# Kernel optimization log

Measured on AMD Instinct MI355X. Metric: run time of the kernel, lower is better.

Reference implementation:

```python
import jax, jax.numpy as jnp
import numpy as np

B, S, D, H, F = 2, 2048, 3072, 32, 8192
DH = D // H  # 96
EPS = 1e-5


def setup_inputs() -> dict:
    key = jax.random.key(0)
    ks = jax.random.split(key, 16)
    sd = 0.02
    inp = {
        "hidden_states": jax.random.normal(ks[0], (B, S, D), jnp.float32),
        "ln1_g": jnp.ones((D,), jnp.float32),
        "ln1_b": jnp.zeros((D,), jnp.float32),
        "Wq": jax.random.normal(ks[1], (D, H, DH), jnp.float32) * sd,
        "bq": jnp.zeros((H, DH), jnp.float32),
        "Wk": jax.random.normal(ks[2], (D, H, DH), jnp.float32) * sd,
        "bk": jnp.zeros((H, DH), jnp.float32),
        "Wv": jax.random.normal(ks[3], (D, H, DH), jnp.float32) * sd,
        "bv": jnp.zeros((H, DH), jnp.float32),
        "Wo": jax.random.normal(ks[4], (H, DH, D), jnp.float32) * sd,
        "bo": jnp.zeros((D,), jnp.float32),
        "ln2_g": jnp.ones((D,), jnp.float32),
        "ln2_b": jnp.zeros((D,), jnp.float32),
        "W1": jax.random.normal(ks[5], (D, F), jnp.float32) * sd,
        "b1": jnp.zeros((F,), jnp.float32),
        "W2": jax.random.normal(ks[6], (F, D), jnp.float32) * sd,
        "b2": jnp.zeros((D,), jnp.float32),
    }
    return inp


def _layernorm(x, g, b):
    m = jnp.mean(x, axis=-1, keepdims=True)
    v = jnp.mean(jnp.square(x - m), axis=-1, keepdims=True)
    return (x - m) * jax.lax.rsqrt(v + EPS) * g + b


def reference(hidden_states, ln1_g, ln1_b, Wq, bq, Wk, bk, Wv, bv, Wo, bo,
              ln2_g, ln2_b, W1, b1, W2, b2):
    # --- LN + self-attention + residual ---
    h = _layernorm(hidden_states, ln1_g, ln1_b)  # [B,S,D]
    q = jnp.einsum('bsd,dhk->bshk', h, Wq) + bq  # [B,S,H,DH]
    k = jnp.einsum('bsd,dhk->bshk', h, Wk) + bk
    v = jnp.einsum('bsd,dhk->bshk', h, Wv) + bv
    scale = 1.0 / np.sqrt(DH).astype(np.float32)
    scores = jnp.einsum('bshk,bthk->bhst', q, k) * scale  # [B,H,S,S]
    attn = jax.nn.softmax(scores, axis=-1)
    ctx = jnp.einsum('bhst,bthk->bshk', attn, v)  # [B,S,H,DH]
    attn_out = jnp.einsum('bshk,hkd->bsd', ctx, Wo) + bo
    h1 = hidden_states + attn_out
    # --- LN + MLP + residual ---
    h2 = _layernorm(h1, ln2_g, ln2_b)
    mlp = jax.nn.gelu(h2 @ W1 + b1, approximate=False) @ W2 + b2
    return h1 + mlp
```

## Files before the change

kernel.cpp:

```cpp
#include <hip/hip_runtime.h>
#include <math.h>

#define DEV __device__ __forceinline__

typedef __attribute__((ext_vector_type(8))) __bf16 bfrag;
typedef __attribute__((ext_vector_type(4))) float f4;
typedef __attribute__((ext_vector_type(8))) unsigned short u16x8;
typedef __attribute__((ext_vector_type(4))) unsigned short u16x4;

DEV unsigned short f2bf(float f) {
  unsigned u = __float_as_uint(f);
  u += 0x7fff + ((u >> 16) & 1);
  return (unsigned short)(u >> 16);
}

DEV void gload_lds16(const void* g, void* l) {
  __builtin_amdgcn_global_load_lds((const __attribute__((address_space(1))) void*)g,
                                   (__attribute__((address_space(3))) void*)l, 16, 0, 0);
}

template<int EPI, int OUTBF, int BIASROW>
__global__ __launch_bounds__(512, 2)
void gemm256(const unsigned short* __restrict__ A,
             const unsigned short* __restrict__ Bt,
             const float* __restrict__ bias,
             const float* __restrict__ res,
             void* __restrict__ outp,
             int M, int N, int K, int gm, int cm, int cn)
{
  __shared__ unsigned short As[2][256 * 64];
  __shared__ unsigned short Bs[2][256 * 64];

  const int tid = threadIdx.x;
  const int lane = tid & 63;
  const int wid = tid >> 6;
  const int wm = wid >> 2, wn = wid & 3;
  const int l15 = lane & 15, lg = lane >> 4;

  const int xcd = blockIdx.x & 7, idx = blockIdx.x >> 3;
  const int cgm = gm / cm;
  const int tm = (xcd % cgm) * cm + idx % cm;
  const int tn = (xcd / cgm) * cn + idx / cm;
  const long tM = (long)tm * 256, tN = (long)tn * 256;

  const int srow = tid >> 3;
  const int lslot = (tid & 7) ^ (srow & 7);
  const unsigned short* aSrc = A + (tM + srow) * (long)K + lslot * 8;
  const unsigned short* bSrc = Bt + (tN + srow) * (long)K + lslot * 8;
  const int NT = K >> 6;

  auto stA = [&](int t, int j) {
    gload_lds16(aSrc + (long)t * 64 + (long)j * 64 * K, &As[t & 1][j * 4096 + tid * 8]);
  };
  auto stB = [&](int t, int j) {
    gload_lds16(bSrc + (long)t * 64 + (long)j * 64 * K, &Bs[t & 1][j * 4096 + tid * 8]);
  };

#pragma unroll
  for (int j = 0; j < 4; ++j) stA(0, j);
#pragma unroll
  for (int j = 0; j < 4; ++j) stB(0, j);
  stA(1, 0); stA(1, 2);
#pragma unroll
  for (int j = 0; j < 4; ++j) stB(1, j);
  asm volatile("s_waitcnt vmcnt(6)" ::: "memory");
  __builtin_amdgcn_s_barrier();

  const int aRow = (wm * 128 + l15) * 64;
  const int bRow = (wn * 64 + l15) * 64;
  const int sx = l15 & 7;
  const int sl0 = ((0 + lg) ^ sx) * 8;
  const int sl1 = ((4 + lg) ^ sx) * 8;

  bfrag aF[4][2], bF[4][2];
  f4 acc[8][4] = {};

  int cur = 0;
  for (int t = 0; t < NT; ++t, cur ^= 1) {
    const unsigned short* Ac = As[cur];
    const unsigned short* Bc = Bs[cur];
    const bool s1 = (t + 1 < NT);
    const bool s2 = (t + 2 < NT);

#pragma unroll
    for (int m = 0; m < 4; ++m) {
      aF[m][0] = *(const bfrag*)&Ac[aRow + m * 1024 + sl0];
      aF[m][1] = *(const bfrag*)&Ac[aRow + m * 1024 + sl1];
    }
#pragma unroll
    for (int n = 0; n < 2; ++n) {
      bF[n][0] = *(const bfrag*)&Bc[bRow + n * 1024 + sl0];
      bF[n][1] = *(const bfrag*)&Bc[bRow + n * 1024 + sl1];
    }
    if (s1) { stA(t + 1, 1); stA(t + 1, 3); }
    __builtin_amdgcn_s_barrier();
    asm volatile("s_waitcnt lgkmcnt(0)" ::: "memory");
    __builtin_amdgcn_s_setprio(1);
#pragma unroll
    for (int m = 0; m < 4; ++m)
#pragma unroll
      for (int n = 0; n < 2; ++n) {
        acc[m][n] = __builtin_amdgcn_mfma_f32_16x16x32_bf16(aF[m][0], bF[n][0], acc[m][n], 0, 0, 0);
        acc[m][n] = __builtin_amdgcn_mfma_f32_16x16x32_bf16(aF[m][1], bF[n][1], acc[m][n], 0, 0, 0);
      }
    __builtin_amdgcn_s_setprio(0);
    __builtin_amdgcn_s_barrier();

#pragma unroll
    for (int n = 2; n < 4; ++n) {
      bF[n][0] = *(const bfrag*)&Bc[bRow + n * 1024 + sl0];
      bF[n][1] = *(const bfrag*)&Bc[bRow + n * 1024 + sl1];
    }
    if (s2) { stA(t + 2, 0); stA(t + 2, 2); }
    __builtin_amdgcn_s_barrier();
    asm volatile("s_waitcnt lgkmcnt(0)" ::: "memory");
    __builtin_amdgcn_s_setprio(1);
#pragma unroll
    for (int m = 0; m < 4; ++m)
#pragma unroll
      for (int n = 2; n < 4; ++n) {
        acc[m][n] = __builtin_amdgcn_mfma_f32_16x16x32_bf16(aF[m][0], bF[n][0], acc[m][n], 0, 0, 0);
        acc[m][n] = __builtin_amdgcn_mfma_f32_16x16x32_bf16(aF[m][1], bF[n][1], acc[m][n], 0, 0, 0);
      }
    __builtin_amdgcn_s_setprio(0);
    __builtin_amdgcn_s_barrier();

#pragma unroll
    for (int m = 0; m < 4; ++m) {
      aF[m][0] = *(const bfrag*)&Ac[aRow + 4096 + m * 1024 + sl0];
      aF[m][1] = *(const bfrag*)&Ac[aRow + 4096 + m * 1024 + sl1];
    }
    if (s2) { stB(t + 2, 0); stB(t + 2, 1); }
    __builtin_amdgcn_s_barrier();
    asm volatile("s_waitcnt lgkmcnt(0)" ::: "memory");
    __builtin_amdgcn_s_setprio(1);
#pragma unroll
    for (int m = 0; m < 4; ++m)
#pragma unroll
      for (int n = 0; n < 2; ++n) {
        acc[4 + m][n] = __builtin_amdgcn_mfma_f32_16x16x32_bf16(aF[m][0], bF[n][0], acc[4 + m][n], 0, 0, 0);
        acc[4 + m][n] = __builtin_amdgcn_mfma_f32_16x16x32_bf16(aF[m][1], bF[n][1], acc[4 + m][n], 0, 0, 0);
      }
    __builtin_amdgcn_s_setprio(0);
    __builtin_amdgcn_s_barrier();

    if (s2) { stB(t + 2, 2); stB(t + 2, 3); }
    __builtin_amdgcn_s_setprio(1);
#pragma unroll
    for (int m = 0; m < 4; ++m)
#pragma unroll
      for (int n = 2; n < 4; ++n) {
        acc[4 + m][n] = __builtin_amdgcn_mfma_f32_16x16x32_bf16(aF[m][0], bF[n][0], acc[4 + m][n], 0, 0, 0);
        acc[4 + m][n] = __builtin_amdgcn_mfma_f32_16x16x32_bf16(aF[m][1], bF[n][1], acc[4 + m][n], 0, 0, 0);
      }
    __builtin_amdgcn_s_setprio(0);
    if (s2)      asm volatile("s_waitcnt vmcnt(6)" ::: "memory");
    else if (s1) asm volatile("s_waitcnt vmcnt(0)" ::: "memory");
    __builtin_amdgcn_s_barrier();
  }

#pragma unroll
  for (int m = 0; m < 8; ++m) {
    const long row0 = tM + wm * 128 + m * 16 + lg * 4;
#pragma unroll
    for (int n = 0; n < 4; ++n) {
      const long col = tN + wn * 64 + n * 16 + l15;
      const float bc = BIASROW ? 0.f : bias[col];
#pragma unroll
      for (int e = 0; e < 4; ++e) {
        const long row = row0 + e;
        float v = acc[m][n][e] + (BIASROW ? bias[row] : bc);
        if constexpr (EPI == 1) v = 0.5f * v * (1.0f + erff(v * 0.70710678118654752f));
        if constexpr (EPI == 2) v += res[row * N + col];
        if constexpr (OUTBF) ((unsigned short*)outp)[row * N + col] = f2bf(v);
        else                 ((float*)outp)[row * N + col] = v;
      }
    }
  }
}

__global__ __launch_bounds__(256)
void ln_bf16(const float* __restrict__ x, const float* __restrict__ g,
             const float* __restrict__ b, unsigned short* __restrict__ out)
{
  __shared__ float red[4];
  const int tid = threadIdx.x;
  const long row = blockIdx.x;
  const float* xr = x + row * 3072;
  float4 v[3];
  float s = 0.f;
#pragma unroll
  for (int i = 0; i < 3; ++i) {
    v[i] = *(const float4*)&xr[i * 1024 + tid * 4];
    s += v[i].x + v[i].y + v[i].z + v[i].w;
  }
#pragma unroll
  for (int o = 32; o > 0; o >>= 1) s += __shfl_xor(s, o);
  if ((tid & 63) == 0) red[tid >> 6] = s;
  __syncthreads();
  s = red[0] + red[1] + red[2] + red[3];
  const float mean = s * (1.f / 3072.f);
  float vs = 0.f;
#pragma unroll
  for (int i = 0; i < 3; ++i) {
    const float dx = v[i].x - mean, dy = v[i].y - mean;
    const float dz = v[i].z - mean, dw = v[i].w - mean;
    vs += dx * dx + dy * dy + dz * dz + dw * dw;
  }
#pragma unroll
  for (int o = 32; o > 0; o >>= 1) vs += __shfl_xor(vs, o);
  __syncthreads();
  if ((tid & 63) == 0) red[tid >> 6] = vs;
  __syncthreads();
  vs = red[0] + red[1] + red[2] + red[3];
  const float rstd = rsqrtf(vs * (1.f / 3072.f) + 1e-5f);
#pragma unroll
  for (int i = 0; i < 3; ++i) {
    const int idx = i * 1024 + tid * 4;
    const float* vp = (const float*)&v[i];
    u16x4 o4;
#pragma unroll
    for (int c = 0; c < 4; ++c)
      o4[c] = f2bf((vp[c] - mean) * rstd * g[idx + c] + b[idx + c]);
    *(u16x4*)&out[row * 3072 + idx] = o4;
  }
}

__global__ __launch_bounds__(256)
void transpose_f32_bf16(const float* __restrict__ in, unsigned short* __restrict__ out,
                        int R, int C)
{
  __shared__ float tile[32][33];
  const int tx = threadIdx.x & 31, ty = threadIdx.x >> 5;
  const long r0 = (long)blockIdx.y * 32, cc0 = (long)blockIdx.x * 32;
#pragma unroll
  for (int i = 0; i < 4; ++i)
    tile[ty + 8 * i][tx] = in[(r0 + ty + 8 * i) * C + cc0 + tx];
  __syncthreads();
#pragma unroll
  for (int i = 0; i < 4; ++i)
    out[(cc0 + ty + 8 * i) * R + r0 + tx] = f2bf(tile[tx][ty + 8 * i]);
}

__global__ __launch_bounds__(256, 3)
void attn_fwd(const unsigned short* __restrict__ qk,
              const unsigned short* __restrict__ vT,
              unsigned short* __restrict__ ctx)
{
  __shared__ unsigned short Qs[64 * 104];
  __shared__ unsigned short Ks[64 * 104];
  __shared__ unsigned short Vt[96 * 72];
  __shared__ unsigned short Ps[4 * 16 * 72];
  const int tid = threadIdx.x;
  const int lane = tid & 63;
  const int w = tid >> 6;
  const int l15 = lane & 15, lg = lane >> 4;
  const int bid = (blockIdx.x & 7) * 256 + (blockIdx.x >> 3);
  const int qb = bid & 31;
  const int h = (bid >> 5) & 31;
  const int b = bid >> 10;
  const long qkbase = ((long)b * 2048) * 6144 + h * 96;
  const long obase  = ((long)b * 2048) * 3072 + h * 96;
  const long vbase  = (long)(h * 96) * 4096 + (long)b * 2048;
  const int qbase = qb * 64;

#pragma unroll
  for (int i = 0; i < 3; ++i) {
    const int c = tid + i * 256;
    const int r = c / 12, c8 = (c % 12) * 8;
    *(u16x8*)&Qs[r * 104 + c8] = *(const u16x8*)&qk[qkbase + (long)(qbase + r) * 6144 + c8];
  }

  float m_run = -1e30f, l_run = 0.f;
  f4 O[6] = {};
  const float sc = 0.1020620726f * 1.4426950409f;

  for (int t = 0; t < 32; ++t) {
    __syncthreads();
    const int kb = t * 64;
#pragma unroll
    for (int i = 0; i < 3; ++i) {
      const int c = tid + i * 256;
      const int r = c / 12, c8 = (c % 12) * 8;
      *(u16x8*)&Ks[r * 104 + c8] = *(const u16x8*)&qk[qkbase + 3072 + (long)(kb + r) * 6144 + c8];
    }
#pragma unroll
    for (int i = 0; i < 3; ++i) {
      const int idx = tid + i * 256;
      const int d = idx >> 3, c8 = (idx & 7) * 8;
      *(u16x8*)&Vt[d * 72 + c8] = *(const u16x8*)&vT[vbase + (long)d * 4096 + kb + c8];
    }
    __syncthreads();

    f4 sf[4];
#pragma unroll
    for (int mb = 0; mb < 4; ++mb) {
      f4 z = {0.f, 0.f, 0.f, 0.f};
      sf[mb] = z;
#pragma unroll
      for (int ks = 0; ks < 3; ++ks) {
        bfrag kf = *(const bfrag*)&Ks[(mb * 16 + l15) * 104 + ks * 32 + lg * 8];
        bfrag qf = *(const bfrag*)&Qs[(w * 16 + l15) * 104 + ks * 32 + lg * 8];
        sf[mb] = __builtin_amdgcn_mfma_f32_16x16x32_bf16(kf, qf, sf[mb], 0, 0, 0);
      }
    }
    float p[16];
    float tmax = -1e30f;
#pragma unroll
    for (int mb = 0; mb < 4; ++mb)
#pragma unroll
      for (int e = 0; e < 4; ++e) {
        const float sv = sf[mb][e] * sc;
        p[mb * 4 + e] = sv;
        tmax = fmaxf(tmax, sv);
      }
    tmax = fmaxf(tmax, __shfl_xor(tmax, 16));
    tmax = fmaxf(tmax, __shfl_xor(tmax, 32));
    const float mnew = fmaxf(m_run, tmax);
    const float alpha = exp2f(m_run - mnew);
    float psum = 0.f;
#pragma unroll
    for (int i = 0; i < 16; ++i) {
      p[i] = exp2f(p[i] - mnew);
      psum += p[i];
    }
    psum += __shfl_xor(psum, 16);
    psum += __shfl_xor(psum, 32);
    l_run = l_run * alpha + psum;
    m_run = mnew;
#pragma unroll
    for (int mb = 0; mb < 4; ++mb) {
      u16x4 pw;
#pragma unroll
      for (int e = 0; e < 4; ++e) pw[e] = f2bf(p[mb * 4 + e]);
      *(u16x4*)&Ps[w * 1152 + l15 * 72 + mb * 16 + lg * 4] = pw;
    }
    float aE[4];
#pragma unroll
    for (int e = 0; e < 4; ++e) aE[e] = __shfl(alpha, lg * 4 + e);
#pragma unroll
    for (int nb = 0; nb < 6; ++nb)
#pragma unroll
      for (int e = 0; e < 4; ++e) O[nb][e] *= aE[e];
#pragma unroll
    for (int nb = 0; nb < 6; ++nb)
#pragma unroll
      for (int ks = 0; ks < 2; ++ks) {
        bfrag pf = *(const bfrag*)&Ps[w * 1152 + l15 * 72 + ks * 32 + lg * 8];
        bfrag vf = *(const bfrag*)&Vt[(nb * 16 + l15) * 72 + ks * 32 + lg * 8];
        O[nb] = __builtin_amdgcn_mfma_f32_16x16x32_bf16(pf, vf, O[nb], 0, 0, 0);
      }
  }
  float lE[4];
#pragma unroll
  for (int e = 0; e < 4; ++e) lE[e] = 1.f / __shfl(l_run, lg * 4 + e);
#pragma unroll
  for (int nb = 0; nb < 6; ++nb)
#pragma unroll
    for (int e = 0; e < 4; ++e) {
      const long row = qbase + w * 16 + lg * 4 + e;
      ctx[obase + row * 3072 + nb * 16 + l15] = f2bf(O[nb][e] * lE[e]);
    }
}

extern "C" void kernel_launch(void* const* d_in, const int* in_sizes, int n_in,
                              void* d_out, int out_size, void* d_ws, size_t ws_size,
                              hipStream_t stream)
{
  (void)in_sizes; (void)n_in; (void)out_size; (void)ws_size;
  const float* x    = (const float*)d_in[0];
  const float* ln1g = (const float*)d_in[1];
  const float* ln1b = (const float*)d_in[2];
  const float* Wq   = (const float*)d_in[3];
  const float* bq   = (const float*)d_in[4];
  const float* Wk   = (const float*)d_in[5];
  const float* bk   = (const float*)d_in[6];
  const float* Wv   = (const float*)d_in[7];
  const float* bv   = (const float*)d_in[8];
  const float* Wo   = (const float*)d_in[9];
  const float* bo   = (const float*)d_in[10];
  const float* ln2g = (const float*)d_in[11];
  const float* ln2b = (const float*)d_in[12];
  const float* W1   = (const float*)d_in[13];
  const float* b1   = (const float*)d_in[14];
  const float* W2   = (const float*)d_in[15];
  const float* b2   = (const float*)d_in[16];

  char* ws = (char*)d_ws;
  unsigned short* WqkT = (unsigned short*)(ws + 0);
  unsigned short* WvT  = (unsigned short*)(ws + 37748736);
  unsigned short* WoT  = (unsigned short*)(ws + 56623104);
  unsigned short* W1T  = (unsigned short*)(ws + 75497472);
  unsigned short* W2T  = (unsigned short*)(ws + 125829120);
  float*          bqk  = (float*)(ws + 176160768);
  unsigned short* hbf  = (unsigned short*)(ws + 176185344);
  unsigned short* ctxb = hbf;
  unsigned short* qkb  = (unsigned short*)(ws + 201351168);
  unsigned short* h2   = qkb;
  unsigned short* act  = (unsigned short*)(ws + 251682816);
  unsigned short* vTb  = (unsigned short*)(ws + 318791680);
  float*          h1   = (float*)d_out;

  const dim3 blk(256);
  const dim3 blk512(512);

  transpose_f32_bf16<<<dim3(96, 96),  blk, 0, stream>>>(Wq, WqkT, 3072, 3072);
  transpose_f32_bf16<<<dim3(96, 96),  blk, 0, stream>>>(Wk, WqkT + 3072 * 3072, 3072, 3072);
  transpose_f32_bf16<<<dim3(96, 96),  blk, 0, stream>>>(Wv, WvT, 3072, 3072);
  transpose_f32_bf16<<<dim3(96, 96),  blk, 0, stream>>>(Wo, WoT, 3072, 3072);
  transpose_f32_bf16<<<dim3(256, 96), blk, 0, stream>>>(W1, W1T, 3072, 8192);
  transpose_f32_bf16<<<dim3(96, 256), blk, 0, stream>>>(W2, W2T, 8192, 3072);
  hipMemcpyAsync(bqk, bq, 3072 * sizeof(float), hipMemcpyDeviceToDevice, stream);
  hipMemcpyAsync(bqk + 3072, bk, 3072 * sizeof(float), hipMemcpyDeviceToDevice, stream);

  ln_bf16<<<4096, blk, 0, stream>>>(x, ln1g, ln1b, hbf);

  gemm256<0, 1, 0><<<384, blk512, 0, stream>>>(hbf, WqkT, bqk, nullptr, qkb, 4096, 6144, 3072, 16, 8, 6);
  gemm256<0, 1, 1><<<192, blk512, 0, stream>>>(WvT, hbf, bv, nullptr, vTb, 3072, 4096, 3072, 12, 6, 4);

  attn_fwd<<<2048, blk, 0, stream>>>(qkb, vTb, ctxb);

  gemm256<2, 0, 0><<<192, blk512, 0, stream>>>(ctxb, WoT, bo, x, h1, 4096, 3072, 3072, 16, 4, 6);

  ln_bf16<<<4096, blk, 0, stream>>>(h1, ln2g, ln2b, h2);

  gemm256<1, 1, 0><<<512, blk512, 0, stream>>>(h2, W1T, b1, nullptr, act, 4096, 8192, 3072, 16, 8, 8);
  gemm256<2, 0, 0><<<192, blk512, 0, stream>>>(act, W2T, b2, h1, (float*)d_out, 4096, 3072, 8192, 16, 4, 6);
}
```

Baseline: 1.255 ms.

## Software-pipeline LDS fragment loads across k-tiles with split register sets in GEMM

Restructures the GEMM main loop so the low A/B fragments for the next k-tile are read from LDS at the end of the current tile. Separate lo/hi fragment registers are kept, and the MFMA quadrants are reordered so fragment reads overlap with compute. The loop is unrolled by two with constant buffer indices and specialized tail iterations, and the explicit lgkmcnt waits are dropped. This aims to hide LDS latency and reduce barrier stalls, at the cost of more fragment registers and more complex vmcnt accounting that could cause occupancy loss or races.

After: 1.367 ms. +8.9%, slower.

```diff
diff --git a/kernel.cpp b/kernel.cpp
--- a/kernel.cpp
+++ b/kernel.cpp
@@ -37,10 +37,10 @@
   const int wm = wid >> 2, wn = wid & 3;
   const int l15 = lane & 15, lg = lane >> 4;
 
-  const int xcd = blockIdx.x & 7, idx = blockIdx.x >> 3;
+  const int xcd = blockIdx.x & 7, bidx = blockIdx.x >> 3;
   const int cgm = gm / cm;
-  const int tm = (xcd % cgm) * cm + idx % cm;
-  const int tn = (xcd / cgm) * cn + idx / cm;
+  const int tm = (xcd % cgm) * cm + bidx % cm;
+  const int tn = (xcd / cgm) * cn + bidx / cm;
   const long tM = (long)tm * 256, tN = (long)tn * 256;
 
   const int srow = tid >> 3;
@@ -72,92 +72,111 @@
   const int sl0 = ((0 + lg) ^ sx) * 8;
   const int sl1 = ((4 + lg) ^ sx) * 8;
 
-  bfrag aF[4][2], bF[4][2];
+  bfrag aLoF[4][2], aHiF[4][2], bLoF[2][2], bHiF[2][2];
   f4 acc[8][4] = {};
 
-  int cur = 0;
-  for (int t = 0; t < NT; ++t, cur ^= 1) {
-    const unsigned short* Ac = As[cur];
-    const unsigned short* Bc = Bs[cur];
-    const bool s1 = (t + 1 < NT);
-    const bool s2 = (t + 2 < NT);
-
-#pragma unroll
-    for (int m = 0; m < 4; ++m) {
-      aF[m][0] = *(const bfrag*)&Ac[aRow + m * 1024 + sl0];
-      aF[m][1] = *(const bfrag*)&Ac[aRow + m * 1024 + sl1];
-    }
-#pragma unroll
-    for (int n = 0; n < 2; ++n) {
-      bF[n][0] = *(const bfrag*)&Bc[bRow + n * 1024 + sl0];
-      bF[n][1] = *(const bfrag*)&Bc[bRow + n * 1024 + sl1];
-    }
-    if (s1) { stA(t + 1, 1); stA(t + 1, 3); }
-    __builtin_amdgcn_s_barrier();
-    asm volatile("s_waitcnt lgkmcnt(0)" ::: "memory");
-    __builtin_amdgcn_s_setprio(1);
-#pragma unroll
-    for (int m = 0; m < 4; ++m)
-#pragma unroll
-      for (int n = 0; n < 2; ++n) {
-        acc[m][n] = __builtin_amdgcn_mfma_f32_16x16x32_bf16(aF[m][0], bF[n][0], acc[m][n], 0, 0, 0);
-        acc[m][n] = __builtin_amdgcn_mfma_f32_16x16x32_bf16(aF[m][1], bF[n][1], acc[m][n], 0, 0, 0);
-      }
-    __builtin_amdgcn_s_setprio(0);
-    __builtin_amdgcn_s_barrier();
-
-#pragma unroll
-    for (int n = 2; n < 4; ++n) {
-      bF[n][0] = *(const bfrag*)&Bc[bRow + n * 1024 + sl0];
-      bF[n][1] = *(const bfrag*)&Bc[bRow + n * 1024 + sl1];
-    }
-    if (s2) { stA(t + 2, 0); stA(t + 2, 2); }
-    __builtin_amdgcn_s_barrier();
-    asm volatile("s_waitcnt lgkmcnt(0)" ::: "memory");
-    __builtin_amdgcn_s_setprio(1);
-#pragma unroll
-    for (int m = 0; m < 4; ++m)
-#pragma unroll
-      for (int n = 2; n < 4; ++n) {
-        acc[m][n] = __builtin_amdgcn_mfma_f32_16x16x32_bf16(aF[m][0], bF[n][0], acc[m][n], 0, 0, 0);
-        acc[m][n] = __builtin_amdgcn_mfma_f32_16x16x32_bf16(aF[m][1], bF[n][1], acc[m][n], 0, 0, 0);
-      }
-    __builtin_amdgcn_s_setprio(0);
-    __builtin_amdgcn_s_barrier();
-
-#pragma unroll
-    for (int m = 0; m < 4; ++m) {
-      aF[m][0] = *(const bfrag*)&Ac[aRow + 4096 + m * 1024 + sl0];
-      aF[m][1] = *(const bfrag*)&Ac[aRow + 4096 + m * 1024 + sl1];
-    }
-    if (s2) { stB(t + 2, 0); stB(t + 2, 1); }
-    __builtin_amdgcn_s_barrier();
-    asm volatile("s_waitcnt lgkmcnt(0)" ::: "memory");
-    __builtin_amdgcn_s_setprio(1);
-#pragma unroll
-    for (int m = 0; m < 4; ++m)
-#pragma unroll
-      for (int n = 0; n < 2; ++n) {
-        acc[4 + m][n] = __builtin_amdgcn_mfma_f32_16x16x32_bf16(aF[m][0], bF[n][0], acc[4 + m][n], 0, 0, 0);
-        acc[4 + m][n] = __builtin_amdgcn_mfma_f32_16x16x32_bf16(aF[m][1], bF[n][1], acc[4 + m][n], 0, 0, 0);
-      }
-    __builtin_amdgcn_s_setprio(0);
-    __builtin_amdgcn_s_barrier();
-
-    if (s2) { stB(t + 2, 2); stB(t + 2, 3); }
-    __builtin_amdgcn_s_setprio(1);
-#pragma unroll
-    for (int m = 0; m < 4; ++m)
-#pragma unroll
-      for (int n = 2; n < 4; ++n) {
-        acc[4 + m][n] = __builtin_amdgcn_mfma_f32_16x16x32_bf16(aF[m][0], bF[n][0], acc[4 + m][n], 0, 0, 0);
-        acc[4 + m][n] = __builtin_amdgcn_mfma_f32_16x16x32_bf16(aF[m][1], bF[n][1], acc[4 + m][n], 0, 0, 0);
-      }
-    __builtin_amdgcn_s_setprio(0);
-    if (s2)      asm volatile("s_waitcnt vmcnt(6)" ::: "memory");
-    else if (s1) asm volatile("s_waitcnt vmcnt(0)" ::: "memory");
-    __builtin_amdgcn_s_barrier();
-  }
+#pragma unroll
+  for (int m = 0; m < 4; ++m) {
+    aLoF[m][0] = *(const bfrag*)&As[0][aRow + m * 1024 + sl0];
+    aLoF[m][1] = *(const bfrag*)&As[0][aRow + m * 1024 + sl1];
+  }
+#pragma unroll
+  for (int n = 0; n < 2; ++n) {
+    bLoF[n][0] = *(const bfrag*)&Bs[0][bRow + n * 1024 + sl0];
+    bLoF[n][1] = *(const bfrag*)&Bs[0][bRow + n * 1024 + sl1];
+  }
+
+#define KTILE(T, CT, MODE)                                                                             \
+  {                                                                                                    \
+    const unsigned short* Ac = (const unsigned short*)As[CT];                                          \
+    const unsigned short* Bc = (const unsigned short*)Bs[CT];                                          \
+                                            \
+    _Pragma("unroll")                                                                                  \
+    for (int n = 0; n < 2; ++n) {                                                                      \
+      bHiF[n][0] = *(const bfrag*)&Bc[bRow + (n + 2) * 1024 + sl0];                                    \
+      bHiF[n][1] = *(const bfrag*)&Bc[bRow + (n + 2) * 1024 + sl1];                                    \
+    }                                                                                                  \
+    if (MODE <= 1) { stA((T) + 1, 1); stA((T) + 1, 3); }                                               \
+    __builtin_amdgcn_s_barrier();                                                                      \
+    __builtin_amdgcn_s_setprio(1);                                                                     \
+    _Pragma("unroll")                                                                                  \
+    for (int m = 0; m < 4; ++m)                                                                        \
+      _Pragma("unroll")                                                                                \
+      for (int n = 0; n < 2; ++n) {                                                                    \
+        acc[m][n] = __builtin_amdgcn_mfma_f32_16x16x32_bf16(aLoF[m][0], bLoF[n][0], acc[m][n], 0, 0, 0); \
+        acc[m][n] = __builtin_amdgcn_mfma_f32_16x16x32_bf16(aLoF[m][1], bLoF[n][1], acc[m][n], 0, 0, 0); \
+      }                                                                                                \
+    __builtin_amdgcn_s_setprio(0);                                                                     \
+    if (MODE == 2) asm volatile("s_waitcnt vmcnt(0)" ::: "memory");                                    \
+    else           asm volatile("s_waitcnt vmcnt(8)" ::: "memory");                                    \
+    __builtin_amdgcn_s_barrier();                                                                      \
+                                                  \
+    _Pragma("unroll")                                                                                  \
+    for (int m = 0; m < 4; ++m) {                                                                      \
+      aHiF[m][0] = *(const bfrag*)&Ac[aRow + 4096 + m * 1024 + sl0];                                   \
+      aHiF[m][1] = *(const bfrag*)&Ac[aRow + 4096 + m * 1024 + sl1];                                   \
+    }                                                                                                  \
+    if (MODE == 0) { stA((T) + 2, 0); stA((T) + 2, 2); }                                               \
+    __builtin_amdgcn_s_barrier();                                                                      \
+    __builtin_amdgcn_s_setprio(1);                                                                     \
+    _Pragma("unroll")                                                                                  \
+    for (int m = 0; m < 4; ++m)                                                                        \
+      _Pragma("unroll")                                                                                \
+      for (int n = 2; n < 4; ++n) {                                                                    \
+        acc[m][n] = __builtin_amdgcn_mfma_f32_16x16x32_bf16(aLoF[m][0], bHiF[n - 2][0], acc[m][n], 0, 0, 0); \
+        acc[m][n] = __builtin_amdgcn_mfma_f32_16x16x32_bf16(aLoF[m][1], bHiF[n - 2][1], acc[m][n], 0, 0, 0); \
+      }                                                                                                \
+    __builtin_amdgcn_s_setprio(0);                                                                     \
+    __builtin_amdgcn_s_barrier();                                                                      \
+                                                                \
+    if (MODE == 0) { stB((T) + 2, 0); stB((T) + 2, 1); }                                               \
+    __builtin_amdgcn_s_barrier();                                                                      \
+    __builtin_amdgcn_s_setprio(1);                                                                     \
+    _Pragma("unroll")                                                                                  \
+    for (int m = 0; m < 4; ++m)                                                                        \
+      _Pragma("unroll")                                                                                \
+      for (int n = 2; n < 4; ++n) {                                                                    \
+        acc[4 + m][n] = __builtin_amdgcn_mfma_f32_16x16x32_bf16(aHiF[m][0], bHiF[n - 2][0], acc[4 + m][n], 0, 0, 0); \
+        acc[4 + m][n] = __builtin_amdgcn_mfma_f32_16x16x32_bf16(aHiF[m][1], bHiF[n - 2][1], acc[4 + m][n], 0, 0, 0); \
+      }                                                                                                \
+    __builtin_amdgcn_s_setprio(0);                                                                     \
+    if (MODE == 0)      asm volatile("s_waitcnt vmcnt(6)" ::: "memory");                               \
+    else if (MODE == 1) asm volatile("s_waitcnt vmcnt(2)" ::: "memory");                               \
+    __builtin_amdgcn_s_barrier();                                                                      \
+                            \
+    if (MODE == 0) { stB((T) + 2, 2); stB((T) + 2, 3); }                                               \
+    __builtin_amdgcn_s_setprio(1);                                                                     \
+    _Pragma("unroll")                                                                                  \
+    for (int m = 0; m < 4; ++m)                                                                        \
+      _Pragma("unroll")                                                                                \
+      for (int n = 0; n < 2; ++n) {                                                                    \
+        acc[4 + m][n] = __builtin_amdgcn_mfma_f32_16x16x32_bf16(aHiF[m][0], bLoF[n][0], acc[4 + m][n], 0, 0, 0); \
+        acc[4 + m][n] = __builtin_amdgcn_mfma_f32_16x16x32_bf16(aHiF[m][1], bLoF[n][1], acc[4 + m][n], 0, 0, 0); \
+      }                                                                                                \
+    __builtin_amdgcn_s_setprio(0);                                                                     \
+    if (MODE != 2) {                                                                                   \
+      const unsigned short* An = (const unsigned short*)As[(CT) ^ 1];                                  \
+      const unsigned short* Bn = (const unsigned short*)Bs[(CT) ^ 1];                                  \
+      _Pragma("unroll")                                                                                \
+      for (int m = 0; m < 4; ++m) {                                                                    \
+        aLoF[m][0] = *(const bfrag*)&An[aRow + m * 1024 + sl0];                                        \
+        aLoF[m][1] = *(const bfrag*)&An[aRow + m * 1024 + sl1];                                        \
+      }                                                                                                \
+      _Pragma("unroll")                                                                                \
+      for (int n = 0; n < 2; ++n) {                                                                    \
+        bLoF[n][0] = *(const bfrag*)&Bn[bRow + n * 1024 + sl0];                                        \
+        bLoF[n][1] = *(const bfrag*)&Bn[bRow + n * 1024 + sl1];                                        \
+      }                                                                                                \
+    }                                                                                                  \
+  }
+
+  for (int t = 0; t < NT - 2; t += 2) {
+    KTILE(t, 0, 0)
+    KTILE(t + 1, 1, 0)
+  }
+  KTILE(NT - 2, 0, 1)
+  KTILE(NT - 1, 1, 2)
+#undef KTILE
 
 #pragma unroll
   for (int m = 0; m < 8; ++m) {
```

## Add 128x128 GEMM kernel for small-grid GEMMs and fuse weight prep launches

Applied to the files above, without the earlier changes.

Adds a 128x128-tile, 256-thread bf16 MFMA GEMM with double-buffered LDS loads and switches the QK, V, Wo and W2 projections to it, raising block counts from 192-384 to 768-1536 so the GPU's compute units are better filled. The six weight transposes and the two bias memcpys are merged into a single prep kernel to cut launch overhead. Smaller tiles lower per-block data reuse, and the LDS layout has no swizzle, which may cause bank conflicts. The epilogue stores scalar elements rather than vectors.

New measurement: 1.211 ms. -3.5%, faster.

```diff
diff --git a/kernel.cpp b/kernel.cpp
--- a/kernel.cpp
+++ b/kernel.cpp
@@ -17,6 +17,89 @@
 DEV void gload_lds16(const void* g, void* l) {
   __builtin_amdgcn_global_load_lds((const __attribute__((address_space(1))) void*)g,
                                    (__attribute__((address_space(3))) void*)l, 16, 0, 0);
+}
+
+template<int EPI, int OUTBF, int BIASROW>
+__global__ __launch_bounds__(256, 2)
+void gemm_bt(const unsigned short* __restrict__ A,
+             const unsigned short* __restrict__ Bt,
+             const float* __restrict__ bias,
+             const float* __restrict__ res,
+             void* __restrict__ outp,
+             int M, int N, int K, int gm, int cm, int cn)
+{
+  __shared__ unsigned short As[2][128 * 32];
+  __shared__ unsigned short Bs[2][128 * 32];
+  const int tid = threadIdx.x;
+  const int lane = tid & 63;
+  const int wid = tid >> 6;
+  const int wr = wid >> 1, wc = wid & 1;
+  const int l15 = lane & 15, lg = lane >> 4;
+
+  const int xcd = blockIdx.x & 7, bidx = blockIdx.x >> 3;
+  const int cgm = gm / cm;
+  const int tm = (xcd % cgm) * cm + bidx % cm;
+  const int tn = (xcd / cgm) * cn + bidx / cm;
+  const long tM = (long)tm * 128;
+  const long tN = (long)tn * 128;
+
+  const int c0 = tid, c1 = tid + 256;
+  const int r0 = c0 >> 2, k0 = (c0 & 3) * 8;
+  const int r1 = c1 >> 2, k1 = (c1 & 3) * 8;
+
+  const unsigned short* A0 = A + (tM + r0) * (long)K + k0;
+  const unsigned short* A1 = A + (tM + r1) * (long)K + k1;
+  const unsigned short* B0 = Bt + (tN + r0) * (long)K + k0;
+  const unsigned short* B1 = Bt + (tN + r1) * (long)K + k1;
+
+  auto stage = [&](int kt, int buf) {
+    const long ko = (long)kt * 32;
+    gload_lds16(A0 + ko, &As[buf][c0 * 8]);
+    gload_lds16(A1 + ko, &As[buf][c1 * 8]);
+    gload_lds16(B0 + ko, &Bs[buf][c0 * 8]);
+    gload_lds16(B1 + ko, &Bs[buf][c1 * 8]);
+  };
+
+  stage(0, 0);
+  f4 acc[4][4] = {};
+  const int nk = K >> 5;
+  int cur = 0;
+  __syncthreads();
+  for (int kt = 0; kt < nk; ++kt) {
+    if (kt + 1 < nk) stage(kt + 1, cur ^ 1);
+    bfrag aF[4], bF[4];
+#pragma unroll
+    for (int m = 0; m < 4; ++m)
+      aF[m] = *(const bfrag*)&As[cur][(wr * 64 + m * 16 + l15) * 32 + lg * 8];
+#pragma unroll
+    for (int n = 0; n < 4; ++n)
+      bF[n] = *(const bfrag*)&Bs[cur][(wc * 64 + n * 16 + l15) * 32 + lg * 8];
+#pragma unroll
+    for (int m = 0; m < 4; ++m)
+#pragma unroll
+      for (int n = 0; n < 4; ++n)
+        acc[m][n] = __builtin_amdgcn_mfma_f32_16x16x32_bf16(aF[m], bF[n], acc[m][n], 0, 0, 0);
+    __syncthreads();
+    cur ^= 1;
+  }
+
+#pragma unroll
+  for (int m = 0; m < 4; ++m) {
+#pragma unroll
+    for (int n = 0; n < 4; ++n) {
+      const long col = tN + wc * 64 + n * 16 + l15;
+      const float bcol = BIASROW ? 0.f : bias[col];
+#pragma unroll
+      for (int e = 0; e < 4; ++e) {
+        const long row = tM + wr * 64 + m * 16 + lg * 4 + e;
+        float v = acc[m][n][e] + (BIASROW ? bias[row] : bcol);
+        if constexpr (EPI == 1) v = 0.5f * v * (1.0f + erff(v * 0.70710678118654752f));
+        if constexpr (EPI == 2) v += res[row * N + col];
+        if constexpr (OUTBF) ((unsigned short*)outp)[row * N + col] = f2bf(v);
+        else                 ((float*)outp)[row * N + col] = v;
+      }
+    }
+  }
 }
 
 template<int EPI, int OUTBF, int BIASROW>
@@ -37,10 +120,10 @@
   const int wm = wid >> 2, wn = wid & 3;
   const int l15 = lane & 15, lg = lane >> 4;
 
-  const int xcd = blockIdx.x & 7, idx = blockIdx.x >> 3;
+  const int xcd = blockIdx.x & 7, bidx = blockIdx.x >> 3;
   const int cgm = gm / cm;
-  const int tm = (xcd % cgm) * cm + idx % cm;
-  const int tn = (xcd / cgm) * cn + idx / cm;
+  const int tm = (xcd % cgm) * cm + bidx % cm;
+  const int tn = (xcd / cgm) * cn + bidx / cm;
   const long tM = (long)tm * 256, tN = (long)tn * 256;
 
   const int srow = tid >> 3;
@@ -227,12 +310,32 @@
 }
 
 __global__ __launch_bounds__(256)
-void transpose_f32_bf16(const float* __restrict__ in, unsigned short* __restrict__ out,
-                        int R, int C)
+void prep_weights(const float* __restrict__ Wq, const float* __restrict__ Wk,
+                  const float* __restrict__ Wv, const float* __restrict__ Wo,
+                  const float* __restrict__ W1, const float* __restrict__ W2,
+                  const float* __restrict__ bq, const float* __restrict__ bk,
+                  unsigned short* __restrict__ WqkT, unsigned short* __restrict__ WvT,
+                  unsigned short* __restrict__ WoT, unsigned short* __restrict__ W1T,
+                  unsigned short* __restrict__ W2T, float* __restrict__ bqk)
 {
   __shared__ float tile[32][33];
+  int bid = blockIdx.x;
+  if (bid < 24) {
+    const int i = bid * 256 + threadIdx.x;
+    bqk[i] = (i < 3072) ? bq[i] : bk[i - 3072];
+    return;
+  }
+  bid -= 24;
+  const float* in; unsigned short* out; int R, C, nbx;
+  if (bid < 9216)        { in = Wq; out = WqkT;                R = 3072; C = 3072; nbx = 96; }
+  else if (bid < 18432)  { in = Wk; out = WqkT + 3072 * 3072;  R = 3072; C = 3072; nbx = 96; bid -= 9216; }
+  else if (bid < 27648)  { in = Wv; out = WvT;                 R = 3072; C = 3072; nbx = 96; bid -= 18432; }
+  else if (bid < 36864)  { in = Wo; out = WoT;                 R = 3072; C = 3072; nbx = 96; bid -= 27648; }
+  else if (bid < 61440)  { in = W1; out = W1T;                 R = 3072; C = 8192; nbx = 256; bid -= 36864; }
+  else                   { in = W2; out = W2T;                 R = 8192; C = 3072; nbx = 96; bid -= 61440; }
+  const int bx = bid % nbx, by = bid / nbx;
   const int tx = threadIdx.x & 31, ty = threadIdx.x >> 5;
-  const long r0 = (long)blockIdx.y * 32, cc0 = (long)blockIdx.x * 32;
+  const long r0 = (long)by * 32, cc0 = (long)bx * 32;
 #pragma unroll
   for (int i = 0; i < 4; ++i)
     tile[ty + 8 * i][tx] = in[(r0 + ty + 8 * i) * C + cc0 + tx];
@@ -404,26 +507,20 @@
   const dim3 blk(256);
   const dim3 blk512(512);
 
-  transpose_f32_bf16<<<dim3(96, 96),  blk, 0, stream>>>(Wq, WqkT, 3072, 3072);
-  transpose_f32_bf16<<<dim3(96, 96),  blk, 0, stream>>>(Wk, WqkT + 3072 * 3072, 3072, 3072);
-  transpose_f32_bf16<<<dim3(96, 96),  blk, 0, stream>>>(Wv, WvT, 3072, 3072);
-  transpose_f32_bf16<<<dim3(96, 96),  blk, 0, stream>>>(Wo, WoT, 3072, 3072);
-  transpose_f32_bf16<<<dim3(256, 96), blk, 0, stream>>>(W1, W1T, 3072, 8192);
-  transpose_f32_bf16<<<dim3(96, 256), blk, 0, stream>>>(W2, W2T, 8192, 3072);
-  hipMemcpyAsync(bqk, bq, 3072 * sizeof(float), hipMemcpyDeviceToDevice, stream);
-  hipMemcpyAsync(bqk + 3072, bk, 3072 * sizeof(float), hipMemcpyDeviceToDevice, stream);
+  prep_weights<<<24 + 86016, blk, 0, stream>>>(Wq, Wk, Wv, Wo, W1, W2, bq, bk,
+                                               WqkT, WvT, WoT, W1T, W2T, bqk);
 
   ln_bf16<<<4096, blk, 0, stream>>>(x, ln1g, ln1b, hbf);
 
-  gemm256<0, 1, 0><<<384, blk512, 0, stream>>>(hbf, WqkT, bqk, nullptr, qkb, 4096, 6144, 3072, 16, 8, 6);
-  gemm256<0, 1, 1><<<192, blk512, 0, stream>>>(WvT, hbf, bv, nullptr, vTb, 3072, 4096, 3072, 12, 6, 4);
+  gemm_bt<0, 1, 0><<<1536, blk, 0, stream>>>(hbf, WqkT, bqk, nullptr, qkb, 4096, 6144, 3072, 32, 16, 12);
+  gemm_bt<0, 1, 1><<<768, blk, 0, stream>>>(WvT, hbf, bv, nullptr, vTb, 3072, 4096, 3072, 24, 12, 8);
 
   attn_fwd<<<2048, blk, 0, stream>>>(qkb, vTb, ctxb);
 
-  gemm256<2, 0, 0><<<192, blk512, 0, stream>>>(ctxb, WoT, bo, x, h1, 4096, 3072, 3072, 16, 4, 6);
+  gemm_bt<2, 0, 0><<<768, blk, 0, stream>>>(ctxb, WoT, bo, x, h1, 4096, 3072, 3072, 32, 16, 6);
 
   ln_bf16<<<4096, blk, 0, stream>>>(h1, ln2g, ln2b, h2);
 
   gemm256<1, 1, 0><<<512, blk512, 0, stream>>>(h2, W1T, b1, nullptr, act, 4096, 8192, 3072, 16, 8, 8);
-  gemm256<2, 0, 0><<<192, blk512, 0, stream>>>(act, W2T, b2, h1, (float*)d_out, 4096, 3072, 8192, 16, 4, 6);
-}
+  gemm_bt<2, 0, 0><<<768, blk, 0, stream>>>(act, W2T, b2, h1, (float*)d_out, 4096, 3072, 8192, 32, 16, 6);
+}
```
